# Performance work log

Measured on AMD Instinct MI355X. Metric: run time of the kernel, lower is better.

## Reference

```python
import jax, jax.numpy as jnp
import numpy as np

B, S, EH, DH, A = 32, 2048, 512, 512, 512

def setup_inputs() -> dict:
    key = jax.random.key(0)
    k1, k2, k3, k4, k5 = jax.random.split(key, 5)
    decoder_hidden = jax.random.normal(k1, (2, B, DH), dtype=jnp.float32)
    encoder_outputs = jax.random.normal(k2, (B, S, 2 * EH), dtype=jnp.float32)
    # Linear weights stored as (in, out) for x @ W convention
    W = jax.random.normal(k3, (2 * EH, A), dtype=jnp.float32) / np.sqrt(2 * EH)
    U = jax.random.normal(k4, (2 * DH, A), dtype=jnp.float32) / np.sqrt(2 * DH)
    v = jax.random.normal(k5, (A, 1), dtype=jnp.float32) / np.sqrt(A)
    return {"decoder_hidden": decoder_hidden, "encoder_outputs": encoder_outputs,
            "W": W, "U": U, "v": v}

def reference(decoder_hidden, encoder_outputs, W, U, v):
    # (2, B, DH) -> (B, 2*DH), matching transpose(0,1).reshape(B, -1)
    b = decoder_hidden.shape[1]
    dh = jnp.transpose(decoder_hidden, (1, 0, 2)).reshape(b, -1)
    temp1 = jnp.einsum('bse,ea->bsa', encoder_outputs, W)   # (B, S, A)
    temp2 = dh @ U                                          # (B, A) — computed once, broadcast over S
    score = jnp.squeeze(jnp.tanh(temp1 + temp2[:, None, :]) @ v, -1)  # (B, S)
    attention_weights = jax.nn.softmax(score, axis=-1)      # (B, S)
    context_vector = jnp.einsum('bs,bse->be', attention_weights, encoder_outputs)[:, None, :]  # (B,1,2EH)
    return context_vector, attention_weights
```

## Files before the change

### kernel.cpp

```cpp
#include <hip/hip_runtime.h>
#include <hip/hip_bf16.h>

#define Bb 32
#define Ss 2048
#define Kk 1024
#define Aa 512

#define BM 64
#define BN 256
#define BK 32
#define NT (Kk / BK)
#define ABUF (BM * BK * 2)
#define BBUF (BN * BK * 2)

typedef __bf16 bf16x8 __attribute__((ext_vector_type(8)));
typedef float f32x4 __attribute__((ext_vector_type(4)));
typedef float f32x8 __attribute__((ext_vector_type(8)));

__device__ __forceinline__ unsigned short f2bf(float f) {
  unsigned u = __float_as_uint(f);
  u += 0x7FFFu + ((u >> 16) & 1u);
  return (unsigned short)(u >> 16);
}

__device__ __forceinline__ float tanh_fast(float x) {
  float e = __expf(2.f * x);
  return (e - 1.f) / (e + 1.f);
}

__device__ __forceinline__ void gll16(const void* g, void* l) {
  __builtin_amdgcn_global_load_lds(
      (const __attribute__((address_space(1))) unsigned int*)g,
      (__attribute__((address_space(3))) unsigned int*)l, 16, 0, 0);
}

__global__ __launch_bounds__(256) void prep_wt(const float* __restrict__ W,
                                               unsigned short* __restrict__ WtT) {
  const int idx = blockIdx.x * 256 + threadIdx.x;
  const int col = idx & 255;
  const int q = (idx >> 8) & 3;
  const int sl = (idx >> 10) & 1;
  const int t = idx >> 11;
  const int k0 = t * 32 + q * 8;
  const int a = sl * 256 + col;
  unsigned short u[8];
#pragma unroll
  for (int j = 0; j < 8; ++j) u[j] = f2bf(W[(size_t)(k0 + j) * Aa + a]);
  uint4 pk;
  pk.x = (unsigned)u[0] | ((unsigned)u[1] << 16);
  pk.y = (unsigned)u[2] | ((unsigned)u[3] << 16);
  pk.z = (unsigned)u[4] | ((unsigned)u[5] << 16);
  pk.w = (unsigned)u[6] | ((unsigned)u[7] << 16);
  *(uint4*)((char*)WtT + (size_t)((t * 2 + sl) * 1024 + q * 256 + col) * 16) = pk;
}

__global__ __launch_bounds__(256) void t2_partial(const float* __restrict__ dh,
                                                  const float* __restrict__ U,
                                                  float* __restrict__ part) {
  const int b = blockIdx.x, kc = blockIdx.y, t = threadIdx.x;
  __shared__ float sdh[128];
  if (t < 128) {
    int k = kc * 128 + t;
    sdh[t] = dh[(k >> 9) * (Bb * 512) + b * 512 + (k & 511)];
  }
  __syncthreads();
#pragma unroll
  for (int h = 0; h < 2; ++h) {
    const int a = h * 256 + t;
    float s = 0.f;
#pragma unroll 8
    for (int kk = 0; kk < 128; ++kk) s += sdh[kk] * U[(size_t)(kc * 128 + kk) * Aa + a];
    part[(size_t)(b * 8 + kc) * Aa + a] = s;
  }
}

__global__ __launch_bounds__(256) void t2_reduce(const float* __restrict__ part,
                                                 float* __restrict__ t2) {
  const int idx = blockIdx.x * 256 + threadIdx.x;
  const int b = idx >> 9, a = idx & 511;
  float s = 0.f;
#pragma unroll
  for (int kc = 0; kc < 8; ++kc) s += part[(size_t)(b * 8 + kc) * Aa + a];
  t2[idx] = s;
}


#define VM(N)                                                                   \
  asm volatile("s_waitcnt vmcnt(" #N ")" ::: "memory");                         \
  __builtin_amdgcn_sched_barrier(0);

#define ALOAD(S, TT)                                                            \
  if ((TT) < NT) {                                                              \
    const float* ap_ = aG + (TT) * BK;                                          \
    areg[S][0] = *(const float4*)ap_;                                           \
    areg[S][1] = *(const float4*)(ap_ + 4);                                     \
  }

#define AWRITE(DST, S)                                                          \
  {                                                                             \
    f32x8 w8_ = {areg[S][0].x, areg[S][0].y, areg[S][0].z, areg[S][0].w,        \
                 areg[S][1].x, areg[S][1].y, areg[S][1].z, areg[S][1].w};       \
    *(bf16x8*)((DST) + a_wb) = __builtin_convertvector(w8_, bf16x8);            \
  }

#define BGLL(TT, DST)                                                           \
  if ((TT) < NT) {                                                              \
    const char* wb_ = wtB + (size_t)((TT) * 2 + slice) * 16384;                 \
    gll16(wb_ + b_c0, (DST) + b_c0);                                            \
    gll16(wb_ + b_c1, (DST) + b_c1);                                            \
    gll16(wb_ + b_c2, (DST) + b_c2);                                            \
    gll16(wb_ + b_c3, (DST) + b_c3);                                            \
  }

#define ITER(AC, BC, AN, SL, SW, T, VMN)                                        \
  {                                                                             \
    bf16x8 af[4], bfr[4];                                                       \
    _Pragma("unroll")                                                           \
    for (int mi = 0; mi < 4; ++mi)                                              \
      af[mi] = *(const bf16x8*)((AC) + (lane >> 4) * 1024 +                     \
                                (mi * 16 + (lane & 15)) * 16);                  \
    _Pragma("unroll")                                                           \
    for (int ni = 0; ni < 4; ++ni)                                              \
      bfr[ni] = *(const bf16x8*)((BC) + (lane >> 4) * 4096 +                    \
                                 (wx * 64 + ni * 16 + (lane & 15)) * 16);       \
    ALOAD(SL, (T) + 2)                                                          \
    __builtin_amdgcn_s_setprio(1);                                              \
    _Pragma("unroll")                                                           \
    for (int mi = 0; mi < 4; ++mi)                                              \
      _Pragma("unroll")                                                         \
      for (int ni = 0; ni < 4; ++ni)                                            \
        acc[mi][ni] = __builtin_amdgcn_mfma_f32_16x16x32_bf16(af[mi], bfr[ni], acc[mi][ni], 0, 0, 0); \
    __builtin_amdgcn_s_setprio(0);                                              \
    __builtin_amdgcn_sched_barrier(0);                                          \
    __builtin_amdgcn_s_barrier();             \
    BGLL((T) + 2, BC)                                                           \
    VM(VMN)                                                                     \
    if ((T) + 1 < NT) { AWRITE(AN, SW) }                                        \
    asm volatile("s_waitcnt lgkmcnt(0)" ::: "memory");                          \
    __builtin_amdgcn_sched_barrier(0);                                          \
    __builtin_amdgcn_s_barrier();                       \
  }

__global__ __launch_bounds__(256, 3) void score_gemm(const float* __restrict__ enc,
                                                     const unsigned short* __restrict__ WtT,
                                                     const float* __restrict__ t2,
                                                     const float* __restrict__ v,
                                                     float* __restrict__ psc) {
  __shared__ __align__(16) char lds[2 * ABUF + 2 * BBUF];
  char* sA0 = lds;
  char* sA1 = lds + ABUF;
  char* sB0 = lds + 2 * ABUF;
  char* sB1 = lds + 2 * ABUF + BBUF;

  const int blk = blockIdx.x;
  const int mtile = blk >> 1, slice = blk & 1;
  const int b = mtile >> 5;
  const float* encF = enc + (size_t)mtile * BM * Kk;
  const char* wtB = (const char*)WtT;

  const int tid = threadIdx.x;
  const int lane = tid & 63;
  const int wx = tid >> 6;

  const int a_row = tid >> 2;
  const int a_q = tid & 3;
  const float* aG = encF + (size_t)a_row * Kk + a_q * 8;
  const int a_wb = a_q * 1024 + a_row * 16;

  const int b_c0 = (0 * 256 + tid) * 16;
  const int b_c1 = (1 * 256 + tid) * 16;
  const int b_c2 = (2 * 256 + tid) * 16;
  const int b_c3 = (3 * 256 + tid) * 16;

  const f32x4 zero = {0.f, 0.f, 0.f, 0.f};
  f32x4 acc[4][4];
#pragma unroll
  for (int i = 0; i < 4; ++i)
#pragma unroll
    for (int j = 0; j < 4; ++j) acc[i][j] = zero;

  float4 areg[2][2];

  {
    ALOAD(0, 0)
    __builtin_amdgcn_sched_barrier(0);
    BGLL(0, sB0)
    __builtin_amdgcn_sched_barrier(0);
    ALOAD(1, 1)
    __builtin_amdgcn_sched_barrier(0);
    BGLL(1, sB1)
    VM(10)
    AWRITE(sA0, 0)
    VM(6)
    asm volatile("s_waitcnt lgkmcnt(0)" ::: "memory");
    __builtin_amdgcn_sched_barrier(0);
    __builtin_amdgcn_s_barrier();
  }

  for (int t = 0; t < 30; t += 2) {
    ITER(sA0, sB0, sA1, 0, 1, t, 6)
    ITER(sA1, sB1, sA0, 1, 0, t + 1, 6)
  }
  ITER(sA0, sB0, sA1, 0, 1, 30, 0)
  ITER(sA1, sB1, sA0, 1, 0, 31, 0)

  float t2v[4], vv[4];
#pragma unroll
  for (int ni = 0; ni < 4; ++ni) {
    int c = slice * BN + wx * 64 + ni * 16 + (lane & 15);
    t2v[ni] = t2[b * Aa + c];
    vv[ni] = v[c];
  }
  float sp[4][4];
#pragma unroll
  for (int mi = 0; mi < 4; ++mi)
#pragma unroll
    for (int j = 0; j < 4; ++j) sp[mi][j] = 0.f;
#pragma unroll
  for (int mi = 0; mi < 4; ++mi)
#pragma unroll
    for (int ni = 0; ni < 4; ++ni)
#pragma unroll
      for (int j = 0; j < 4; ++j) {
        float x = acc[mi][ni][j] + t2v[ni];
        sp[mi][j] += vv[ni] * tanh_fast(x);
      }

  float* sbuf = (float*)lds;
#pragma unroll
  for (int mi = 0; mi < 4; ++mi)
#pragma unroll
    for (int j = 0; j < 4; ++j) {
      float s = sp[mi][j];
      s += __shfl_xor(s, 1);
      s += __shfl_xor(s, 2);
      s += __shfl_xor(s, 4);
      s += __shfl_xor(s, 8);
      if ((lane & 15) == 0) {
        int r = mi * 16 + ((lane >> 4) << 2) + j;
        sbuf[r * 4 + wx] = s;
      }
    }
  __syncthreads();
  if (tid < BM) {
    float s = sbuf[tid * 4] + sbuf[tid * 4 + 1] + sbuf[tid * 4 + 2] + sbuf[tid * 4 + 3];
    psc[slice * 65536 + mtile * BM + tid] = s;
  }
}

__global__ __launch_bounds__(256) void softmax_k(const float* __restrict__ psc,
                                                 float* __restrict__ aw) {
  const int b = blockIdx.x, t = threadIdx.x;
  __shared__ float red[8];
  float s[8];
  float m = -3.4e38f;
#pragma unroll
  for (int i = 0; i < 8; ++i) {
    int idx = b * Ss + t + i * 256;
    s[i] = psc[idx] + psc[65536 + idx];
    m = fmaxf(m, s[i]);
  }
#pragma unroll
  for (int off = 1; off < 64; off <<= 1) m = fmaxf(m, __shfl_xor(m, off));
  const int lane = t & 63, wv = t >> 6;
  if (lane == 0) red[wv] = m;
  __syncthreads();
  m = fmaxf(fmaxf(red[0], red[1]), fmaxf(red[2], red[3]));
  float e[8];
  float l = 0.f;
#pragma unroll
  for (int i = 0; i < 8; ++i) { e[i] = __expf(s[i] - m); l += e[i]; }
#pragma unroll
  for (int off = 1; off < 64; off <<= 1) l += __shfl_xor(l, off);
  if (lane == 0) red[4 + wv] = l;
  __syncthreads();
  l = red[4] + red[5] + red[6] + red[7];
  const float inv = 1.f / l;
#pragma unroll
  for (int i = 0; i < 8; ++i) aw[b * Ss + t + i * 256] = e[i] * inv;
}

__global__ __launch_bounds__(256) void ctx_partial(const float* __restrict__ enc,
                                                   const float* __restrict__ aw,
                                                   float* __restrict__ part) {
  const int b = blockIdx.x, ch = blockIdx.y, t = threadIdx.x;
  __shared__ float sw[64];
  const int s0 = ch * 64;
  if (t < 64) sw[t] = aw[b * Ss + s0 + t];
  __syncthreads();
  float ax = 0.f, ay = 0.f, az = 0.f, aww = 0.f;
  const float* ebase = enc + (size_t)(b * Ss + s0) * Kk + t * 4;
#pragma unroll 4
  for (int r = 0; r < 64; ++r) {
    const float4 ev = *(const float4*)(ebase + (size_t)r * Kk);
    const float w = sw[r];
    ax += w * ev.x; ay += w * ev.y; az += w * ev.z; aww += w * ev.w;
  }
  float4 o; o.x = ax; o.y = ay; o.z = az; o.w = aww;
  *(float4*)(part + (size_t)(b * 32 + ch) * Kk + t * 4) = o;
}

__global__ __launch_bounds__(256) void ctx_reduce(const float* __restrict__ part,
                                                  float* __restrict__ ctx) {
  const int idx = blockIdx.x * 256 + threadIdx.x;
  const int b = idx >> 10, e = idx & 1023;
  float s = 0.f;
#pragma unroll
  for (int ch = 0; ch < 32; ++ch) s += part[(size_t)(b * 32 + ch) * Kk + e];
  ctx[idx] = s;
}

extern "C" void kernel_launch(void* const* d_in, const int* in_sizes, int n_in,
                              void* d_out, int out_size, void* d_ws, size_t ws_size,
                              hipStream_t stream) {
  const float* dh  = (const float*)d_in[0];
  const float* enc = (const float*)d_in[1];
  const float* W   = (const float*)d_in[2];
  const float* U   = (const float*)d_in[3];
  const float* v   = (const float*)d_in[4];

  float* out_ctx = (float*)d_out;
  float* out_aw  = (float*)d_out + 32768;

  char* ws = (char*)d_ws;
  unsigned short* WtT = (unsigned short*)ws;
  float* t2p   = (float*)(ws + 1048576);
  float* t2    = (float*)(ws + 1048576 + 524288);
  float* cpart = (float*)(ws + 1048576 + 524288 + 65536);
  float* psc   = (float*)(ws + 1048576 + 524288 + 65536 + 4194304);

  prep_wt<<<256, 256, 0, stream>>>(W, WtT);
  t2_partial<<<dim3(32, 8), 256, 0, stream>>>(dh, U, t2p);
  t2_reduce<<<64, 256, 0, stream>>>(t2p, t2);
  score_gemm<<<2048, 256, 0, stream>>>(enc, WtT, t2, v, psc);
  softmax_k<<<32, 256, 0, stream>>>(psc, out_aw);
  ctx_partial<<<dim3(32, 32), 256, 0, stream>>>(enc, out_aw, cpart);
  ctx_reduce<<<128, 256, 0, stream>>>(cpart, out_ctx);
}
```

Measured before the change: 179.8 us.

## Drop LDS staging; load MFMA fragments directly from global into registers

Removes the shared-memory double-buffered pipeline for both the encoder tile and the bf16 weight tile. Each wave now loads its own A fragments (fp32, converted to bf16 in registers) and B fragments straight from global memory, with register-level prefetching and no block barriers. This eliminates LDS traffic and syncs, but each of the four waves now reads the full A tile separately, giving four times the global/L2 reads of A. It also raises register pressure, so launch bounds drop occupancy from 3 to 2 blocks per SIMD.

New measurement: 334.8 us. 1.86x slower.

```diff
diff --git a/kernel.cpp b/kernel.cpp
--- a/kernel.cpp
+++ b/kernel.cpp
@@ -10,8 +10,6 @@
 #define BN 256
 #define BK 32
 #define NT (Kk / BK)
-#define ABUF (BM * BK * 2)
-#define BBUF (BN * BK * 2)
 
 typedef __bf16 bf16x8 __attribute__((ext_vector_type(8)));
 typedef float f32x4 __attribute__((ext_vector_type(4)));
@@ -26,12 +24,6 @@
 __device__ __forceinline__ float tanh_fast(float x) {
   float e = __expf(2.f * x);
   return (e - 1.f) / (e + 1.f);
-}
-
-__device__ __forceinline__ void gll16(const void* g, void* l) {
-  __builtin_amdgcn_global_load_lds(
-      (const __attribute__((address_space(1))) unsigned int*)g,
-      (__attribute__((address_space(3))) unsigned int*)l, 16, 0, 0);
 }
 
 __global__ __launch_bounds__(256) void prep_wt(const float* __restrict__ W,
@@ -85,92 +77,69 @@
 }
 
 
-#define VM(N)                                                                   \
-  asm volatile("s_waitcnt vmcnt(" #N ")" ::: "memory");                         \
-  __builtin_amdgcn_sched_barrier(0);
-
-#define ALOAD(S, TT)                                                            \
+#define ALOAD(TT)                                                               \
   if ((TT) < NT) {                                                              \
-    const float* ap_ = aG + (TT) * BK;                                          \
-    areg[S][0] = *(const float4*)ap_;                                           \
-    areg[S][1] = *(const float4*)(ap_ + 4);                                     \
-  }
-
-#define AWRITE(DST, S)                                                          \
+    const float* ap_ = aBase + (TT) * BK;                                       \
+    areg[0] = *(const float4*)(ap_);                                            \
+    areg[1] = *(const float4*)(ap_ + 4);                                        \
+    areg[2] = *(const float4*)(ap_ + 16384);                                    \
+    areg[3] = *(const float4*)(ap_ + 16388);                                    \
+    areg[4] = *(const float4*)(ap_ + 32768);                                    \
+    areg[5] = *(const float4*)(ap_ + 32772);                                    \
+    areg[6] = *(const float4*)(ap_ + 49152);                                    \
+    areg[7] = *(const float4*)(ap_ + 49156);                                    \
+  }
+
+#define BLOAD(S, TT)                                                            \
+  if ((TT) < NT) {                                                              \
+    const char* bp_ = bBase + (size_t)(TT) * 32768;                             \
+    breg[S][0] = *(const bf16x8*)(bp_);                                         \
+    breg[S][1] = *(const bf16x8*)(bp_ + 256);                                   \
+    breg[S][2] = *(const bf16x8*)(bp_ + 512);                                   \
+    breg[S][3] = *(const bf16x8*)(bp_ + 768);                                   \
+  }
+
+#define ITER(CUR, T)                                                            \
   {                                                                             \
-    f32x8 w8_ = {areg[S][0].x, areg[S][0].y, areg[S][0].z, areg[S][0].w,        \
-                 areg[S][1].x, areg[S][1].y, areg[S][1].z, areg[S][1].w};       \
-    *(bf16x8*)((DST) + a_wb) = __builtin_convertvector(w8_, bf16x8);            \
-  }
-
-#define BGLL(TT, DST)                                                           \
-  if ((TT) < NT) {                                                              \
-    const char* wb_ = wtB + (size_t)((TT) * 2 + slice) * 16384;                 \
-    gll16(wb_ + b_c0, (DST) + b_c0);                                            \
-    gll16(wb_ + b_c1, (DST) + b_c1);                                            \
-    gll16(wb_ + b_c2, (DST) + b_c2);                                            \
-    gll16(wb_ + b_c3, (DST) + b_c3);                                            \
-  }
-
-#define ITER(AC, BC, AN, SL, SW, T, VMN)                                        \
-  {                                                                             \
-    bf16x8 af[4], bfr[4];                                                       \
+    bf16x8 af[4];                                                               \
     _Pragma("unroll")                                                           \
-    for (int mi = 0; mi < 4; ++mi)                                              \
-      af[mi] = *(const bf16x8*)((AC) + (lane >> 4) * 1024 +                     \
-                                (mi * 16 + (lane & 15)) * 16);                  \
-    _Pragma("unroll")                                                           \
-    for (int ni = 0; ni < 4; ++ni)                                              \
-      bfr[ni] = *(const bf16x8*)((BC) + (lane >> 4) * 4096 +                    \
-                                 (wx * 64 + ni * 16 + (lane & 15)) * 16);       \
-    ALOAD(SL, (T) + 2)                                                          \
+    for (int mi = 0; mi < 4; ++mi) {                                            \
+      f32x8 w8_ = {areg[2 * mi].x,     areg[2 * mi].y,                          \
+                   areg[2 * mi].z,     areg[2 * mi].w,                          \
+                   areg[2 * mi + 1].x, areg[2 * mi + 1].y,                      \
+                   areg[2 * mi + 1].z, areg[2 * mi + 1].w};                     \
+      af[mi] = __builtin_convertvector(w8_, bf16x8);                            \
+    }                                                                           \
+    ALOAD((T) + 1)                                                              \
     __builtin_amdgcn_s_setprio(1);                                              \
     _Pragma("unroll")                                                           \
     for (int mi = 0; mi < 4; ++mi)                                              \
       _Pragma("unroll")                                                         \
       for (int ni = 0; ni < 4; ++ni)                                            \
-        acc[mi][ni] = __builtin_amdgcn_mfma_f32_16x16x32_bf16(af[mi], bfr[ni], acc[mi][ni], 0, 0, 0); \
+        acc[mi][ni] = __builtin_amdgcn_mfma_f32_16x16x32_bf16(af[mi], breg[CUR][ni], acc[mi][ni], 0, 0, 0); \
     __builtin_amdgcn_s_setprio(0);                                              \
-    __builtin_amdgcn_sched_barrier(0);                                          \
-    __builtin_amdgcn_s_barrier();             \
-    BGLL((T) + 2, BC)                                                           \
-    VM(VMN)                                                                     \
-    if ((T) + 1 < NT) { AWRITE(AN, SW) }                                        \
-    asm volatile("s_waitcnt lgkmcnt(0)" ::: "memory");                          \
-    __builtin_amdgcn_sched_barrier(0);                                          \
-    __builtin_amdgcn_s_barrier();                       \
-  }
-
-__global__ __launch_bounds__(256, 3) void score_gemm(const float* __restrict__ enc,
+    BLOAD(CUR, (T) + 2)                                                         \
+  }
+
+__global__ __launch_bounds__(256, 2) void score_gemm(const float* __restrict__ enc,
                                                      const unsigned short* __restrict__ WtT,
                                                      const float* __restrict__ t2,
                                                      const float* __restrict__ v,
                                                      float* __restrict__ psc) {
-  __shared__ __align__(16) char lds[2 * ABUF + 2 * BBUF];
-  char* sA0 = lds;
-  char* sA1 = lds + ABUF;
-  char* sB0 = lds + 2 * ABUF;
-  char* sB1 = lds + 2 * ABUF + BBUF;
+  __shared__ float sbuf[BM * 4];
 
   const int blk = blockIdx.x;
   const int mtile = blk >> 1, slice = blk & 1;
   const int b = mtile >> 5;
-  const float* encF = enc + (size_t)mtile * BM * Kk;
-  const char* wtB = (const char*)WtT;
-
   const int tid = threadIdx.x;
   const int lane = tid & 63;
   const int wx = tid >> 6;
 
-  const int a_row = tid >> 2;
-  const int a_q = tid & 3;
-  const float* aG = encF + (size_t)a_row * Kk + a_q * 8;
-  const int a_wb = a_q * 1024 + a_row * 16;
-
-  const int b_c0 = (0 * 256 + tid) * 16;
-  const int b_c1 = (1 * 256 + tid) * 16;
-  const int b_c2 = (2 * 256 + tid) * 16;
-  const int b_c3 = (3 * 256 + tid) * 16;
+  const float* aBase = enc + (size_t)mtile * BM * Kk
+                       + (size_t)(lane & 15) * Kk + (lane >> 4) * 8;
+
+  const char* bBase = (const char*)WtT + (size_t)slice * 16384
+                      + ((lane >> 4) * 256 + wx * 64 + (lane & 15)) * 16;
 
   const f32x4 zero = {0.f, 0.f, 0.f, 0.f};
   f32x4 acc[4][4];
@@ -179,30 +148,17 @@
 #pragma unroll
     for (int j = 0; j < 4; ++j) acc[i][j] = zero;
 
-  float4 areg[2][2];
-
-  {
-    ALOAD(0, 0)
-    __builtin_amdgcn_sched_barrier(0);
-    BGLL(0, sB0)
-    __builtin_amdgcn_sched_barrier(0);
-    ALOAD(1, 1)
-    __builtin_amdgcn_sched_barrier(0);
-    BGLL(1, sB1)
-    VM(10)
-    AWRITE(sA0, 0)
-    VM(6)
-    asm volatile("s_waitcnt lgkmcnt(0)" ::: "memory");
-    __builtin_amdgcn_sched_barrier(0);
-    __builtin_amdgcn_s_barrier();
-  }
-
-  for (int t = 0; t < 30; t += 2) {
-    ITER(sA0, sB0, sA1, 0, 1, t, 6)
-    ITER(sA1, sB1, sA0, 1, 0, t + 1, 6)
-  }
-  ITER(sA0, sB0, sA1, 0, 1, 30, 0)
-  ITER(sA1, sB1, sA0, 1, 0, 31, 0)
+  float4 areg[8];
+  bf16x8 breg[2][4];
+
+  ALOAD(0)
+  BLOAD(0, 0)
+  BLOAD(1, 1)
+
+  for (int t = 0; t < NT; t += 2) {
+    ITER(0, t)
+    ITER(1, t + 1)
+  }
 
   float t2v[4], vv[4];
 #pragma unroll
@@ -226,7 +182,6 @@
         sp[mi][j] += vv[ni] * tanh_fast(x);
       }
 
-  float* sbuf = (float*)lds;
 #pragma unroll
   for (int mi = 0; mi < 4; ++mi)
 #pragma unroll
```
